# Optimization experiments

Hardware: AMD Instinct MI355X
Metric: run time of the kernel (lower is better)

Reference implementation:

```python
import jax, jax.numpy as jnp
import numpy as np

B, T, D = 8, 4096, 512
Q, K = 4, 1024
KERNEL, STRIDE = 5, 2
COMMIT = 0.25


def setup_inputs() -> dict:
    key = jax.random.key(0)
    k1, k2, k3 = jax.random.split(key, 3)
    x = jax.random.normal(k1, (B, T, D), dtype=jnp.float32)
    codebooks = jax.random.normal(k2, (Q, K, D), dtype=jnp.float32)
    # he_normal fan_in = KERNEL * D
    conv_w = jax.random.normal(k3, (KERNEL, D, D), dtype=jnp.float32) * np.sqrt(2.0 / (KERNEL * D))
    return {"x": x, "codebooks": codebooks, "conv_w": conv_w}


def _vq_nearest(residual, cb):
    # residual: [B,T,D], cb: [K,D] -> squared L2 distances [B,T,K]
    d = (jnp.sum(residual * residual, axis=-1, keepdims=True)
         - 2.0 * jnp.einsum('btd,kd->btk', residual, cb)
         + jnp.sum(cb * cb, axis=-1))
    idx = jnp.argmin(d, axis=-1)          # [B,T] int
    q = cb[idx]                            # [B,T,D] gather
    return q, idx


def residual_vq(x, codebooks):
    residual = x
    quantized_out = jnp.zeros_like(x)
    losses = []
    indices = []
    for qi in range(Q):  # small fixed number of quantizers
        q, idx = _vq_nearest(residual, codebooks[qi])
        # commitment loss (codebook frozen at inference / EMA-updated in training)
        losses.append(COMMIT * jnp.mean((jax.lax.stop_gradient(q) - residual) ** 2))
        # straight-through estimator
        q_st = residual + jax.lax.stop_gradient(q - residual)
        quantized_out = quantized_out + q_st
        residual = residual - jax.lax.stop_gradient(q)
        indices.append(idx)
    loss = jnp.sum(jnp.stack(losses))
    return quantized_out, jnp.stack(indices, axis=0), loss


def reference(x, codebooks, conv_w):
    quantized_out, indices, vq_loss = residual_vq(x, codebooks)
    # Conv1D, stride 2, 'same' padding, no bias: NWC x WIO -> NWC
    y = jax.lax.conv_general_dilated(
        quantized_out, conv_w,
        window_strides=(STRIDE,), padding='SAME',
        dimension_numbers=('NWC', 'WIO', 'NWC'))
    y = jax.nn.gelu(y, approximate=False)
    return y, quantized_out, indices, vq_loss
```

## Files before the change

kernel.cpp:

```cpp
#include <hip/hip_runtime.h>
#include <math.h>

#define Bq 8
#define Tq 4096
#define Dq 512
#define Qn 4
#define Kk 1024
#define OWn 2048
#define NROWS (Bq*Tq)

#define QO_OFF (Bq*OWn*Dq)
#define IDX_OFF (QO_OFF + Bq*Tq*Dq)
#define LOSS_OFF (IDX_OFF + Qn*NROWS)

typedef __bf16 bf16x8 __attribute__((ext_vector_type(8)));
typedef _Float16 f16x8 __attribute__((ext_vector_type(8)));
typedef float f32x16 __attribute__((ext_vector_type(16)));
typedef float f32x4 __attribute__((ext_vector_type(4)));

__device__ __forceinline__ unsigned pack2h(_Float16 a, _Float16 b) {
  return (unsigned)__builtin_bit_cast(unsigned short, a)
       | ((unsigned)__builtin_bit_cast(unsigned short, b) << 16);
}

__global__ __launch_bounds__(256) void prep_cb(const float* __restrict__ cb,
                                               float* __restrict__ cbnorm,
                                               _Float16* __restrict__ cbf,
                                               float* __restrict__ lacc) {
  int w = threadIdx.x >> 6, lane = threadIdx.x & 63;
  int row = blockIdx.x * 4 + w;
  int q = row >> 10, k = row & 1023;
  const f32x4* c4 = (const f32x4*)(cb + (size_t)row * Dq);
  f32x4 v0 = c4[lane * 2], v1 = c4[lane * 2 + 1];
  float s = v0.x*v0.x + v0.y*v0.y + v0.z*v0.z + v0.w*v0.w
          + v1.x*v1.x + v1.y*v1.y + v1.z*v1.z + v1.w*v1.w;
  f16x8 bv;
  bv[0]=(_Float16)v0.x; bv[1]=(_Float16)v0.y; bv[2]=(_Float16)v0.z; bv[3]=(_Float16)v0.w;
  bv[4]=(_Float16)v1.x; bv[5]=(_Float16)v1.y; bv[6]=(_Float16)v1.z; bv[7]=(_Float16)v1.w;
  int ds = lane >> 1, hs = lane & 1;
  size_t off = ((size_t)((k >> 5) * 32 + ds) * 2 + hs) * 256 + (k & 31) * 8;
  *(f16x8*)(cbf + (size_t)q * (Kk * Dq) + off) = bv;
#pragma unroll
  for (int off2 = 32; off2; off2 >>= 1) s += __shfl_down(s, off2);
  if (lane == 0) cbnorm[row] = s;
  if (blockIdx.x == 0 && threadIdx.x == 0) *lacc = 0.f;
}

__global__ __launch_bounds__(256) void prep_cmax(const float* __restrict__ cbnorm,
                                                 float* __restrict__ cmax) {
  int w = threadIdx.x >> 6, lane = threadIdx.x & 63;
  float m = 0.f;
#pragma unroll
  for (int j = 0; j < 16; ++j) m = fmaxf(m, cbnorm[w * Kk + lane * 16 + j]);
#pragma unroll
  for (int off = 32; off; off >>= 1) m = fmaxf(m, __shfl_down(m, off));
  if (lane == 0) cmax[w] = sqrtf(m);
}

__global__ __launch_bounds__(256) void prep_wb(const float* __restrict__ w,
                                               __bf16* __restrict__ wb) {
  int g = blockIdx.x * 256 + threadIdx.x;
  int l31 = g & 31, hs = (g >> 5) & 1, c32 = (g >> 6) & 15, s = g >> 10;
  int kw = s >> 5, ci16 = s & 31;
  int ci = ci16 * 16 + hs * 8;
  int co = c32 * 32 + l31;
  bf16x8 bv;
#pragma unroll
  for (int e = 0; e < 8; ++e)
    bv[e] = (__bf16)w[(size_t)(kw * Dq + ci + e) * Dq + co];
  *(bf16x8*)(wb + (size_t)g * 8) = bv;
}

__global__ __launch_bounds__(512, 1) void vq_all(
    const float* __restrict__ x, float* __restrict__ qo,
    const _Float16* __restrict__ cbf, const float* __restrict__ cb,
    const float* __restrict__ cbnorm, const float* __restrict__ cmax,
    float* __restrict__ idxo, float* __restrict__ lacc) {
  __shared__ _Float16 rh[64 * 512];
  __shared__ unsigned redB[64 * 8];
  __shared__ float rnorm_l[64];
  __shared__ float thrL[64];
  __shared__ int rowcount[64];
  __shared__ unsigned short rowlist[64 * 32];

  const int tid = threadIdx.x;
  const int w = tid >> 6, lane = tid & 63, l31 = lane & 31, hs = lane >> 5;
  const int row0g = blockIdx.x * 64;
  char* rhc = (char*)rh;

  f32x4 r0[8], r1[8];
#pragma unroll
  for (int rr = 0; rr < 8; ++rr) {
    size_t gb = (size_t)(row0g + w * 8 + rr) * Dq + lane * 8;
    r0[rr] = *(const f32x4*)(x + gb);
    r1[rr] = *(const f32x4*)(x + gb + 4);
  }
  float lsum = 0.f;

#pragma unroll 1
  for (int qi = 0; qi < Qn; ++qi) {
    const _Float16* cbf_q = cbf + (size_t)qi * (Kk * Dq);
    const float*    cb_q  = cb  + (size_t)qi * (Kk * Dq);
    const float*    cbn_q = cbnorm + qi * Kk;

#pragma unroll
    for (int rr = 0; rr < 8; ++rr) {
      int row = w * 8 + rr;
      f16x8 bv;
      bv[0]=(_Float16)r0[rr].x; bv[1]=(_Float16)r0[rr].y;
      bv[2]=(_Float16)r0[rr].z; bv[3]=(_Float16)r0[rr].w;
      bv[4]=(_Float16)r1[rr].x; bv[5]=(_Float16)r1[rr].y;
      bv[6]=(_Float16)r1[rr].z; bv[7]=(_Float16)r1[rr].w;
      *(f16x8*)(rhc + ((row * 1024 + lane * 16) ^ ((row & 7) << 4))) = bv;
      float rn = r0[rr].x*r0[rr].x + r0[rr].y*r0[rr].y + r0[rr].z*r0[rr].z + r0[rr].w*r0[rr].w
               + r1[rr].x*r1[rr].x + r1[rr].y*r1[rr].y + r1[rr].z*r1[rr].z + r1[rr].w*r1[rr].w;
#pragma unroll
      for (int off = 1; off < 64; off <<= 1) rn += __shfl_xor(rn, off);
      if (lane == 0) rnorm_l[row] = rn;
    }
    __syncthreads();

    unsigned psA[4][8], psB[4][8];
    const int ab0 = l31 * 1024 + hs * 16;
    const int asw = (l31 & 7) << 4;
#pragma unroll
    for (int p = 0; p < 2; ++p) {
      const int ct0 = 2 * p, ct1 = 2 * p + 1;
      const _Float16* bp0 = cbf_q + (size_t)(w * 4 + ct0) * 16384 + hs * 256 + l31 * 8;
      const _Float16* bp1 = cbf_q + (size_t)(w * 4 + ct1) * 16384 + hs * 256 + l31 * 8;
      f32x16 a00, a01, a10, a11;
#pragma unroll
      for (int i = 0; i < 16; ++i) { a00[i]=0.f; a01[i]=0.f; a10[i]=0.f; a11[i]=0.f; }
#pragma unroll 8
      for (int ds = 0; ds < 32; ++ds) {
        f16x8 a0 = *(const f16x8*)(rhc + ((ab0 + ds * 32) ^ asw));
        f16x8 a1 = *(const f16x8*)(rhc + ((ab0 + 32 * 1024 + ds * 32) ^ asw));
        f16x8 b0 = *(const f16x8*)(bp0 + ds * 512);
        f16x8 b1 = *(const f16x8*)(bp1 + ds * 512);
        a00 = __builtin_amdgcn_mfma_f32_32x32x16_f16(a0, b0, a00, 0, 0, 0);
        a01 = __builtin_amdgcn_mfma_f32_32x32x16_f16(a0, b1, a01, 0, 0, 0);
        a10 = __builtin_amdgcn_mfma_f32_32x32x16_f16(a1, b0, a10, 0, 0, 0);
        a11 = __builtin_amdgcn_mfma_f32_32x32x16_f16(a1, b1, a11, 0, 0, 0);
      }
      const float cn0 = cbn_q[w * 128 + ct0 * 32 + l31];
      const float cn1 = cbn_q[w * 128 + ct1 * 32 + l31];
#pragma unroll
      for (int j = 0; j < 8; ++j) {
        psA[ct0][j] = pack2h((_Float16)(cn0 - 2.f * a00[2*j]), (_Float16)(cn0 - 2.f * a00[2*j+1]));
        psA[ct1][j] = pack2h((_Float16)(cn1 - 2.f * a01[2*j]), (_Float16)(cn1 - 2.f * a01[2*j+1]));
        psB[ct0][j] = pack2h((_Float16)(cn0 - 2.f * a10[2*j]), (_Float16)(cn0 - 2.f * a10[2*j+1]));
        psB[ct1][j] = pack2h((_Float16)(cn1 - 2.f * a11[2*j]), (_Float16)(cn1 - 2.f * a11[2*j+1]));
      }
    }

#pragma unroll
    for (int rt = 0; rt < 2; ++rt) {
      unsigned pk[16];
#pragma unroll
      for (int i = 0; i < 16; ++i) {
        pk[i] = 0xFFFFFFFFu;
#pragma unroll
        for (int ct = 0; ct < 4; ++ct) {
          unsigned col = (unsigned)(w * 128 + ct * 32 + l31);
          unsigned u = ((rt == 0 ? psA[ct][i >> 1] : psB[ct][i >> 1]) >> ((i & 1) * 16)) & 0xFFFFu;
          unsigned key = (u & 0x8000u) ? (u ^ 0xFFFFu) : (u | 0x8000u);
          unsigned pkc = (key << 10) | col;
          if (pkc < pk[i]) pk[i] = pkc;
        }
#pragma unroll
        for (int off = 1; off <= 16; off <<= 1) {
          unsigned t = __shfl_xor(pk[i], off);
          if (t < pk[i]) pk[i] = t;
        }
      }
      if (l31 == 0) {
#pragma unroll
        for (int i = 0; i < 16; ++i) {
          int rit = rt * 32 + (i & 3) + 8 * (i >> 2) + 4 * hs;
          redB[rit * 8 + w] = pk[i];
        }
      }
    }
    __syncthreads();

    if (tid < 64) {
      unsigned mb = redB[tid * 8];
#pragma unroll
      for (int j = 1; j < 8; ++j) {
        unsigned v = redB[tid * 8 + j];
        if (v < mb) mb = v;
      }
      unsigned key = (mb >> 10) & 0xFFFFu;
      unsigned ub = (key & 0x8000u) ? (key ^ 0x8000u) : (key ^ 0xFFFFu);
      float mstar = (float)__builtin_bit_cast(_Float16, (unsigned short)ub);
      float rn = sqrtf(rnorm_l[tid]);
      float cm = cmax[qi];
      thrL[tid] = mstar + 0.005f * rn * cm + 0.001f * fabsf(mstar) + 0.3f;
      rowcount[tid] = 0;
    }
    __syncthreads();

#pragma unroll
    for (int rt = 0; rt < 2; ++rt) {
#pragma unroll
      for (int i = 0; i < 16; ++i) {
        int rit = rt * 32 + (i & 3) + 8 * (i >> 2) + 4 * hs;
        float t = thrL[rit];
#pragma unroll
        for (int ct = 0; ct < 4; ++ct) {
          unsigned col = (unsigned)(w * 128 + ct * 32 + l31);
          unsigned u = ((rt == 0 ? psA[ct][i >> 1] : psB[ct][i >> 1]) >> ((i & 1) * 16)) & 0xFFFFu;
          float s = (float)__builtin_bit_cast(_Float16, (unsigned short)u);
          if (s <= t) {
            int p = atomicAdd(&rowcount[rit], 1);
            if (p < 32) rowlist[rit * 32 + p] = (unsigned short)col;
          }
        }
      }
    }
    __syncthreads();

#pragma unroll
    for (int rr = 0; rr < 8; ++rr) {
      int row = w * 8 + rr;
      int cnt = rowcount[row];
      int bk;
      if (cnt == 1) {
        bk = (int)rowlist[row * 32];
      } else {
        int total = (cnt > 32) ? Kk : cnt;
        float bs = 3.4028235e38f; bk = 1 << 30;
        for (int ci2 = 0; ci2 < total; ++ci2) {
          int k = (cnt > 32) ? ci2 : (int)rowlist[row * 32 + ci2];
          const f32x4* crow = (const f32x4*)(cb_q + ((size_t)k << 9)) + lane * 2;
          f32x4 c0 = crow[0], c1 = crow[1];
          float dot = 0.f;
          dot = fmaf(r0[rr].x, c0.x, dot); dot = fmaf(r0[rr].y, c0.y, dot);
          dot = fmaf(r0[rr].z, c0.z, dot); dot = fmaf(r0[rr].w, c0.w, dot);
          dot = fmaf(r1[rr].x, c1.x, dot); dot = fmaf(r1[rr].y, c1.y, dot);
          dot = fmaf(r1[rr].z, c1.z, dot); dot = fmaf(r1[rr].w, c1.w, dot);
#pragma unroll
          for (int off = 1; off < 64; off <<= 1) dot += __shfl_xor(dot, off);
          float sc = cbn_q[k] - 2.f * dot;
          if (sc < bs || (sc == bs && k < bk)) { bs = sc; bk = k; }
        }
      }
      if (lane == 0) idxo[(size_t)qi * NROWS + row0g + row] = (float)bk;
      const f32x4* crow = (const f32x4*)(cb_q + ((size_t)bk << 9)) + lane * 2;
      f32x4 c0 = crow[0], c1 = crow[1];
      r0[rr].x -= c0.x; r0[rr].y -= c0.y; r0[rr].z -= c0.z; r0[rr].w -= c0.w;
      r1[rr].x -= c1.x; r1[rr].y -= c1.y; r1[rr].z -= c1.z; r1[rr].w -= c1.w;
      lsum += r0[rr].x*r0[rr].x + r0[rr].y*r0[rr].y + r0[rr].z*r0[rr].z + r0[rr].w*r0[rr].w
            + r1[rr].x*r1[rr].x + r1[rr].y*r1[rr].y + r1[rr].z*r1[rr].z + r1[rr].w*r1[rr].w;
    }
    __syncthreads();
  }

#pragma unroll
  for (int rr = 0; rr < 8; ++rr) {
    size_t gb = (size_t)(row0g + w * 8 + rr) * Dq + lane * 8;
    f32x4 xv0 = *(const f32x4*)(x + gb), xv1 = *(const f32x4*)(x + gb + 4);
    f32x4 o0, o1;
    o0.x = xv0.x - r0[rr].x; o0.y = xv0.y - r0[rr].y;
    o0.z = xv0.z - r0[rr].z; o0.w = xv0.w - r0[rr].w;
    o1.x = xv1.x - r1[rr].x; o1.y = xv1.y - r1[rr].y;
    o1.z = xv1.z - r1[rr].z; o1.w = xv1.w - r1[rr].w;
    *(f32x4*)(qo + gb) = o0;
    *(f32x4*)(qo + gb + 4) = o1;
  }
#pragma unroll
  for (int off = 1; off < 64; off <<= 1) lsum += __shfl_xor(lsum, off);
  if (lane == 0) atomicAdd(lacc, lsum);
}

__global__ __launch_bounds__(512, 2) void conv_mfma(const float* __restrict__ qo,
                                                    const __bf16* __restrict__ wb,
                                                    float* __restrict__ y) {
  __shared__ char As[259 * 128];
  const int tid = threadIdx.x;
  const int w = tid >> 6, lane = tid & 63, l31 = lane & 31, hs = lane >> 5;
  const int rowblk = blockIdx.x, coblk = blockIdx.y;
  const int n = rowblk >> 4;
  const int o0 = (rowblk & 15) * 128;
  const int t0 = 2 * o0 - 1;
  const int c32g = coblk * 8 + w;

  f32x16 acc[4];
#pragma unroll
  for (int rt = 0; rt < 4; ++rt)
#pragma unroll
    for (int i = 0; i < 16; ++i) acc[rt][i] = 0.f;

  for (int ct8 = 0; ct8 < 8; ++ct8) {
    __syncthreads();
    for (int s = tid; s < 2072; s += 512) {
      int irow = s >> 3, cg = s & 7;
      int t = t0 + irow;
      bf16x8 bv;
      if (t >= 0 && t < Tq) {
        const float* src = qo + ((size_t)(n * Tq + t)) * Dq + ct8 * 64 + cg * 8;
        f32x4 v0 = *(const f32x4*)(src), v1 = *(const f32x4*)(src + 4);
        bv[0]=(__bf16)v0.x; bv[1]=(__bf16)v0.y; bv[2]=(__bf16)v0.z; bv[3]=(__bf16)v0.w;
        bv[4]=(__bf16)v1.x; bv[5]=(__bf16)v1.y; bv[6]=(__bf16)v1.z; bv[7]=(__bf16)v1.w;
      } else {
#pragma unroll
        for (int e = 0; e < 8; ++e) bv[e] = (__bf16)0.f;
      }
      *(bf16x8*)(As + ((irow * 128 + cg * 16) ^ (((irow >> 1) & 7) << 4))) = bv;
    }
    __syncthreads();
#pragma unroll
    for (int kw = 0; kw < 5; ++kw) {
#pragma unroll
      for (int ks = 0; ks < 4; ++ks) {
        int s16 = kw * 32 + ct8 * 4 + ks;
        bf16x8 b = *(const bf16x8*)(wb + ((size_t)(s16 * 16 + c32g) * 2 + hs) * 256 + l31 * 8);
#pragma unroll
        for (int rt = 0; rt < 4; ++rt) {
          int ir = 2 * (rt * 32 + l31) + kw;
          bf16x8 a = *(const bf16x8*)(As + ((ir * 128 + ks * 32 + hs * 16) ^ (((ir >> 1) & 7) << 4)));
          acc[rt] = __builtin_amdgcn_mfma_f32_32x32x16_bf16(a, b, acc[rt], 0, 0, 0);
        }
      }
    }
  }
  const int co = coblk * 256 + w * 32 + l31;
#pragma unroll
  for (int rt = 0; rt < 4; ++rt)
#pragma unroll
    for (int i = 0; i < 16; ++i) {
      int orow = rt * 32 + (i & 3) + 8 * (i >> 2) + 4 * hs;
      float v = acc[rt][i];
      float g = 0.5f * v * (1.f + erff(v * 0.70710678118654752f));
      y[((size_t)(n * OWn + o0 + orow)) * Dq + co] = g;
    }
}

__global__ void loss_final(const float* __restrict__ lacc, float* __restrict__ out) {
  out[0] = 0.25f * lacc[0] / 16777216.0f;
}

extern "C" void kernel_launch(void* const* d_in, const int* in_sizes, int n_in,
                              void* d_out, int out_size, void* d_ws, size_t ws_size,
                              hipStream_t stream) {
  const float* x  = (const float*)d_in[0];
  const float* cb = (const float*)d_in[1];
  const float* cw = (const float*)d_in[2];
  float* out = (float*)d_out;
  float* y    = out;
  float* qo   = out + QO_OFF;
  float* idxo = out + IDX_OFF;
  float* losso = out + LOSS_OFF;

  float* fws    = (float*)d_ws;
  float* lacc   = fws;
  float* cmax   = fws + 8;
  float* cbnorm = fws + 16;
  _Float16* cbf = (_Float16*)((char*)d_ws + (32 << 10));
  __bf16* wb  = (__bf16*)((char*)d_ws + (8 << 20));

  prep_cb<<<1024, 256, 0, stream>>>(cb, cbnorm, cbf, lacc);
  prep_cmax<<<1, 256, 0, stream>>>(cbnorm, cmax);
  prep_wb<<<640, 256, 0, stream>>>(cw, wb);

  vq_all<<<512, 512, 0, stream>>>(x, qo, cbf, cb, cbnorm, cmax, idxo, lacc);

  conv_mfma<<<dim3(128, 2), 512, 0, stream>>>(qo, wb, y);
  loss_final<<<1, 1, 0, stream>>>(lacc, losso);
}
```

Before: 478.5 us.

## Recompute distance GEMM in second pass instead of holding packed scores in registers

Replaces the stored 64 packed-half score registers and the packed-key argmin reduction with a running packed-f16 min per row, followed by a second full MFMA pass that recomputes the scores for candidate thresholding. This cuts register pressure and the key-packing ALU work, but doubles the codebook-distance matmul work and the codebook loads per quantizer. The thresholding now compares fp32 scores rather than the f16-rounded ones.

```diff
diff --git a/kernel.cpp b/kernel.cpp
--- a/kernel.cpp
+++ b/kernel.cpp
@@ -21,6 +21,15 @@
 __device__ __forceinline__ unsigned pack2h(_Float16 a, _Float16 b) {
   return (unsigned)__builtin_bit_cast(unsigned short, a)
        | ((unsigned)__builtin_bit_cast(unsigned short, b) << 16);
+}
+__device__ __forceinline__ unsigned pmin2h(unsigned a, unsigned b) {
+  _Float16 al = __builtin_bit_cast(_Float16, (unsigned short)(a & 0xFFFFu));
+  _Float16 ah = __builtin_bit_cast(_Float16, (unsigned short)(a >> 16));
+  _Float16 bl = __builtin_bit_cast(_Float16, (unsigned short)(b & 0xFFFFu));
+  _Float16 bh = __builtin_bit_cast(_Float16, (unsigned short)(b >> 16));
+  _Float16 ml = al < bl ? al : bl;
+  _Float16 mh = ah < bh ? ah : bh;
+  return pack2h(ml, mh);
 }
 
 __global__ __launch_bounds__(256) void prep_cb(const float* __restrict__ cb,
@@ -77,7 +86,7 @@
     const float* __restrict__ cbnorm, const float* __restrict__ cmax,
     float* __restrict__ idxo, float* __restrict__ lacc) {
   __shared__ _Float16 rh[64 * 512];
-  __shared__ unsigned redB[64 * 8];
+  __shared__ float minW[64 * 8];
   __shared__ float rnorm_l[64];
   __shared__ float thrL[64];
   __shared__ int rowcount[64];
@@ -120,101 +129,94 @@
     }
     __syncthreads();
 
-    unsigned psA[4][8], psB[4][8];
     const int ab0 = l31 * 1024 + hs * 16;
+    const int ab1 = ab0 + 32 * 1024;
     const int asw = (l31 & 7) << 4;
-#pragma unroll
-    for (int p = 0; p < 2; ++p) {
-      const int ct0 = 2 * p, ct1 = 2 * p + 1;
-      const _Float16* bp0 = cbf_q + (size_t)(w * 4 + ct0) * 16384 + hs * 256 + l31 * 8;
-      const _Float16* bp1 = cbf_q + (size_t)(w * 4 + ct1) * 16384 + hs * 256 + l31 * 8;
-      f32x16 a00, a01, a10, a11;
-#pragma unroll
-      for (int i = 0; i < 16; ++i) { a00[i]=0.f; a01[i]=0.f; a10[i]=0.f; a11[i]=0.f; }
+
+    unsigned minp[16];
+#pragma unroll
+    for (int i = 0; i < 16; ++i) minp[i] = 0x7C007C00u;
+
+#pragma unroll 1
+    for (int ct = 0; ct < 4; ++ct) {
+      const int col = w * 128 + ct * 32 + l31;
+      const _Float16* bp = cbf_q + (size_t)(w * 4 + ct) * 16384 + hs * 256 + l31 * 8;
+      f32x16 acc0, acc1;
+#pragma unroll
+      for (int i = 0; i < 16; ++i) { acc0[i] = 0.f; acc1[i] = 0.f; }
 #pragma unroll 8
       for (int ds = 0; ds < 32; ++ds) {
         f16x8 a0 = *(const f16x8*)(rhc + ((ab0 + ds * 32) ^ asw));
-        f16x8 a1 = *(const f16x8*)(rhc + ((ab0 + 32 * 1024 + ds * 32) ^ asw));
-        f16x8 b0 = *(const f16x8*)(bp0 + ds * 512);
-        f16x8 b1 = *(const f16x8*)(bp1 + ds * 512);
-        a00 = __builtin_amdgcn_mfma_f32_32x32x16_f16(a0, b0, a00, 0, 0, 0);
-        a01 = __builtin_amdgcn_mfma_f32_32x32x16_f16(a0, b1, a01, 0, 0, 0);
-        a10 = __builtin_amdgcn_mfma_f32_32x32x16_f16(a1, b0, a10, 0, 0, 0);
-        a11 = __builtin_amdgcn_mfma_f32_32x32x16_f16(a1, b1, a11, 0, 0, 0);
-      }
-      const float cn0 = cbn_q[w * 128 + ct0 * 32 + l31];
-      const float cn1 = cbn_q[w * 128 + ct1 * 32 + l31];
-#pragma unroll
-      for (int j = 0; j < 8; ++j) {
-        psA[ct0][j] = pack2h((_Float16)(cn0 - 2.f * a00[2*j]), (_Float16)(cn0 - 2.f * a00[2*j+1]));
-        psA[ct1][j] = pack2h((_Float16)(cn1 - 2.f * a01[2*j]), (_Float16)(cn1 - 2.f * a01[2*j+1]));
-        psB[ct0][j] = pack2h((_Float16)(cn0 - 2.f * a10[2*j]), (_Float16)(cn0 - 2.f * a10[2*j+1]));
-        psB[ct1][j] = pack2h((_Float16)(cn1 - 2.f * a11[2*j]), (_Float16)(cn1 - 2.f * a11[2*j+1]));
-      }
-    }
-
-#pragma unroll
-    for (int rt = 0; rt < 2; ++rt) {
-      unsigned pk[16];
+        f16x8 a1 = *(const f16x8*)(rhc + ((ab1 + ds * 32) ^ asw));
+        f16x8 b  = *(const f16x8*)(bp + ds * 512);
+        acc0 = __builtin_amdgcn_mfma_f32_32x32x16_f16(a0, b, acc0, 0, 0, 0);
+        acc1 = __builtin_amdgcn_mfma_f32_32x32x16_f16(a1, b, acc1, 0, 0, 0);
+      }
+      const float cn = cbn_q[col];
 #pragma unroll
       for (int i = 0; i < 16; ++i) {
-        pk[i] = 0xFFFFFFFFu;
-#pragma unroll
-        for (int ct = 0; ct < 4; ++ct) {
-          unsigned col = (unsigned)(w * 128 + ct * 32 + l31);
-          unsigned u = ((rt == 0 ? psA[ct][i >> 1] : psB[ct][i >> 1]) >> ((i & 1) * 16)) & 0xFFFFu;
-          unsigned key = (u & 0x8000u) ? (u ^ 0xFFFFu) : (u | 0x8000u);
-          unsigned pkc = (key << 10) | col;
-          if (pkc < pk[i]) pk[i] = pkc;
-        }
-#pragma unroll
-        for (int off = 1; off <= 16; off <<= 1) {
-          unsigned t = __shfl_xor(pk[i], off);
-          if (t < pk[i]) pk[i] = t;
-        }
-      }
-      if (l31 == 0) {
-#pragma unroll
-        for (int i = 0; i < 16; ++i) {
-          int rit = rt * 32 + (i & 3) + 8 * (i >> 2) + 4 * hs;
-          redB[rit * 8 + w] = pk[i];
-        }
+        _Float16 h0 = (_Float16)(cn - 2.f * acc0[i]);
+        _Float16 h1 = (_Float16)(cn - 2.f * acc1[i]);
+        minp[i] = pmin2h(minp[i], pack2h(h0, h1));
+      }
+    }
+#pragma unroll
+    for (int i = 0; i < 16; ++i) {
+#pragma unroll
+      for (int off = 1; off <= 16; off <<= 1)
+        minp[i] = pmin2h(minp[i], __shfl_xor(minp[i], off));
+    }
+    if (l31 == 0) {
+#pragma unroll
+      for (int i = 0; i < 16; ++i) {
+        int rit = (i & 3) + 8 * (i >> 2) + 4 * hs;
+        minW[rit * 8 + w] =
+            (float)__builtin_bit_cast(_Float16, (unsigned short)(minp[i] & 0xFFFFu));
+        minW[(rit + 32) * 8 + w] =
+            (float)__builtin_bit_cast(_Float16, (unsigned short)(minp[i] >> 16));
       }
     }
     __syncthreads();
 
     if (tid < 64) {
-      unsigned mb = redB[tid * 8];
-#pragma unroll
-      for (int j = 1; j < 8; ++j) {
-        unsigned v = redB[tid * 8 + j];
-        if (v < mb) mb = v;
-      }
-      unsigned key = (mb >> 10) & 0xFFFFu;
-      unsigned ub = (key & 0x8000u) ? (key ^ 0x8000u) : (key ^ 0xFFFFu);
-      float mstar = (float)__builtin_bit_cast(_Float16, (unsigned short)ub);
+      float m = minW[tid * 8];
+#pragma unroll
+      for (int j = 1; j < 8; ++j) m = fminf(m, minW[tid * 8 + j]);
       float rn = sqrtf(rnorm_l[tid]);
       float cm = cmax[qi];
-      thrL[tid] = mstar + 0.005f * rn * cm + 0.001f * fabsf(mstar) + 0.3f;
+      thrL[tid] = m + 0.005f * rn * cm + 0.001f * fabsf(m) + 0.3f;
       rowcount[tid] = 0;
     }
     __syncthreads();
 
-#pragma unroll
-    for (int rt = 0; rt < 2; ++rt) {
+#pragma unroll 1
+    for (int ct = 0; ct < 4; ++ct) {
+      const int col = w * 128 + ct * 32 + l31;
+      const _Float16* bp = cbf_q + (size_t)(w * 4 + ct) * 16384 + hs * 256 + l31 * 8;
+      f32x16 acc0, acc1;
+#pragma unroll
+      for (int i = 0; i < 16; ++i) { acc0[i] = 0.f; acc1[i] = 0.f; }
+#pragma unroll 8
+      for (int ds = 0; ds < 32; ++ds) {
+        f16x8 a0 = *(const f16x8*)(rhc + ((ab0 + ds * 32) ^ asw));
+        f16x8 a1 = *(const f16x8*)(rhc + ((ab1 + ds * 32) ^ asw));
+        f16x8 b  = *(const f16x8*)(bp + ds * 512);
+        acc0 = __builtin_amdgcn_mfma_f32_32x32x16_f16(a0, b, acc0, 0, 0, 0);
+        acc1 = __builtin_amdgcn_mfma_f32_32x32x16_f16(a1, b, acc1, 0, 0, 0);
+      }
+      const float cn = cbn_q[col];
 #pragma unroll
       for (int i = 0; i < 16; ++i) {
-        int rit = rt * 32 + (i & 3) + 8 * (i >> 2) + 4 * hs;
-        float t = thrL[rit];
-#pragma unroll
-        for (int ct = 0; ct < 4; ++ct) {
-          unsigned col = (unsigned)(w * 128 + ct * 32 + l31);
-          unsigned u = ((rt == 0 ? psA[ct][i >> 1] : psB[ct][i >> 1]) >> ((i & 1) * 16)) & 0xFFFFu;
-          float s = (float)__builtin_bit_cast(_Float16, (unsigned short)u);
-          if (s <= t) {
-            int p = atomicAdd(&rowcount[rit], 1);
-            if (p < 32) rowlist[rit * 32 + p] = (unsigned short)col;
-          }
+        int rit = (i & 3) + 8 * (i >> 2) + 4 * hs;
+        float s0 = cn - 2.f * acc0[i];
+        float s1 = cn - 2.f * acc1[i];
+        if (s0 <= thrL[rit]) {
+          int p = atomicAdd(&rowcount[rit], 1);
+          if (p < 32) rowlist[rit * 32 + p] = (unsigned short)col;
+        }
+        if (s1 <= thrL[rit + 32]) {
+          int p = atomicAdd(&rowcount[rit + 32], 1);
+          if (p < 32) rowlist[(rit + 32) * 32 + p] = (unsigned short)col;
         }
       }
     }
```

Measured after the change: 531.5 us. 1.11x slower.

## Stream residual through global qo instead of holding it in registers; split MFMA tiles

Applied to the files above, without the earlier changes.

Drops the 64 per-thread registers that held the residual across all quantizer passes. Each pass now recomputes the residual as x minus the running quantized sum, which is read back from and written to the qo output in global memory. The distance MMA is also restructured to run the two row tiles one after another, so only two 16-wide accumulators are live instead of four. The aim is to cut register pressure, likely to avoid spills or free VGPRs, at the cost of extra global reads and writes of x and qo on every pass.

```diff
diff --git a/kernel.cpp b/kernel.cpp
--- a/kernel.cpp
+++ b/kernel.cpp
@@ -87,14 +87,6 @@
   const int w = tid >> 6, lane = tid & 63, l31 = lane & 31, hs = lane >> 5;
   const int row0g = blockIdx.x * 64;
   char* rhc = (char*)rh;
-
-  f32x4 r0[8], r1[8];
-#pragma unroll
-  for (int rr = 0; rr < 8; ++rr) {
-    size_t gb = (size_t)(row0g + w * 8 + rr) * Dq + lane * 8;
-    r0[rr] = *(const f32x4*)(x + gb);
-    r1[rr] = *(const f32x4*)(x + gb + 4);
-  }
   float lsum = 0.f;
 
 #pragma unroll 1
@@ -103,17 +95,26 @@
     const float*    cb_q  = cb  + (size_t)qi * (Kk * Dq);
     const float*    cbn_q = cbnorm + qi * Kk;
 
-#pragma unroll
+#pragma unroll 1
     for (int rr = 0; rr < 8; ++rr) {
       int row = w * 8 + rr;
+      size_t gb = (size_t)(row0g + row) * Dq + lane * 8;
+      f32x4 xv0 = *(const f32x4*)(x + gb), xv1 = *(const f32x4*)(x + gb + 4);
+      f32x4 qv0 = {0.f,0.f,0.f,0.f}, qv1 = {0.f,0.f,0.f,0.f};
+      if (qi != 0) { qv0 = *(const f32x4*)(qo + gb); qv1 = *(const f32x4*)(qo + gb + 4); }
+      f32x4 rv0, rv1;
+      rv0.x = xv0.x - qv0.x; rv0.y = xv0.y - qv0.y;
+      rv0.z = xv0.z - qv0.z; rv0.w = xv0.w - qv0.w;
+      rv1.x = xv1.x - qv1.x; rv1.y = xv1.y - qv1.y;
+      rv1.z = xv1.z - qv1.z; rv1.w = xv1.w - qv1.w;
       f16x8 bv;
-      bv[0]=(_Float16)r0[rr].x; bv[1]=(_Float16)r0[rr].y;
-      bv[2]=(_Float16)r0[rr].z; bv[3]=(_Float16)r0[rr].w;
-      bv[4]=(_Float16)r1[rr].x; bv[5]=(_Float16)r1[rr].y;
-      bv[6]=(_Float16)r1[rr].z; bv[7]=(_Float16)r1[rr].w;
+      bv[0]=(_Float16)rv0.x; bv[1]=(_Float16)rv0.y;
+      bv[2]=(_Float16)rv0.z; bv[3]=(_Float16)rv0.w;
+      bv[4]=(_Float16)rv1.x; bv[5]=(_Float16)rv1.y;
+      bv[6]=(_Float16)rv1.z; bv[7]=(_Float16)rv1.w;
       *(f16x8*)(rhc + ((row * 1024 + lane * 16) ^ ((row & 7) << 4))) = bv;
-      float rn = r0[rr].x*r0[rr].x + r0[rr].y*r0[rr].y + r0[rr].z*r0[rr].z + r0[rr].w*r0[rr].w
-               + r1[rr].x*r1[rr].x + r1[rr].y*r1[rr].y + r1[rr].z*r1[rr].z + r1[rr].w*r1[rr].w;
+      float rn = rv0.x*rv0.x + rv0.y*rv0.y + rv0.z*rv0.z + rv0.w*rv0.w
+               + rv1.x*rv1.x + rv1.y*rv1.y + rv1.z*rv1.z + rv1.w*rv1.w;
 #pragma unroll
       for (int off = 1; off < 64; off <<= 1) rn += __shfl_xor(rn, off);
       if (lane == 0) rnorm_l[row] = rn;
@@ -128,28 +129,31 @@
       const int ct0 = 2 * p, ct1 = 2 * p + 1;
       const _Float16* bp0 = cbf_q + (size_t)(w * 4 + ct0) * 16384 + hs * 256 + l31 * 8;
       const _Float16* bp1 = cbf_q + (size_t)(w * 4 + ct1) * 16384 + hs * 256 + l31 * 8;
-      f32x16 a00, a01, a10, a11;
-#pragma unroll
-      for (int i = 0; i < 16; ++i) { a00[i]=0.f; a01[i]=0.f; a10[i]=0.f; a11[i]=0.f; }
-#pragma unroll 8
-      for (int ds = 0; ds < 32; ++ds) {
-        f16x8 a0 = *(const f16x8*)(rhc + ((ab0 + ds * 32) ^ asw));
-        f16x8 a1 = *(const f16x8*)(rhc + ((ab0 + 32 * 1024 + ds * 32) ^ asw));
-        f16x8 b0 = *(const f16x8*)(bp0 + ds * 512);
-        f16x8 b1 = *(const f16x8*)(bp1 + ds * 512);
-        a00 = __builtin_amdgcn_mfma_f32_32x32x16_f16(a0, b0, a00, 0, 0, 0);
-        a01 = __builtin_amdgcn_mfma_f32_32x32x16_f16(a0, b1, a01, 0, 0, 0);
-        a10 = __builtin_amdgcn_mfma_f32_32x32x16_f16(a1, b0, a10, 0, 0, 0);
-        a11 = __builtin_amdgcn_mfma_f32_32x32x16_f16(a1, b1, a11, 0, 0, 0);
-      }
       const float cn0 = cbn_q[w * 128 + ct0 * 32 + l31];
       const float cn1 = cbn_q[w * 128 + ct1 * 32 + l31];
 #pragma unroll
-      for (int j = 0; j < 8; ++j) {
-        psA[ct0][j] = pack2h((_Float16)(cn0 - 2.f * a00[2*j]), (_Float16)(cn0 - 2.f * a00[2*j+1]));
-        psA[ct1][j] = pack2h((_Float16)(cn1 - 2.f * a01[2*j]), (_Float16)(cn1 - 2.f * a01[2*j+1]));
-        psB[ct0][j] = pack2h((_Float16)(cn0 - 2.f * a10[2*j]), (_Float16)(cn0 - 2.f * a10[2*j+1]));
-        psB[ct1][j] = pack2h((_Float16)(cn1 - 2.f * a11[2*j]), (_Float16)(cn1 - 2.f * a11[2*j+1]));
+      for (int rt = 0; rt < 2; ++rt) {
+        f32x16 acc0, acc1;
+#pragma unroll
+        for (int i = 0; i < 16; ++i) { acc0[i] = 0.f; acc1[i] = 0.f; }
+        const int abase = ab0 + rt * 32768;
+#pragma unroll 8
+        for (int ds = 0; ds < 32; ++ds) {
+          f16x8 a  = *(const f16x8*)(rhc + ((abase + ds * 32) ^ asw));
+          f16x8 b0 = *(const f16x8*)(bp0 + ds * 512);
+          f16x8 b1 = *(const f16x8*)(bp1 + ds * 512);
+          acc0 = __builtin_amdgcn_mfma_f32_32x32x16_f16(a, b0, acc0, 0, 0, 0);
+          acc1 = __builtin_amdgcn_mfma_f32_32x32x16_f16(a, b1, acc1, 0, 0, 0);
+        }
+#pragma unroll
+        for (int j = 0; j < 8; ++j) {
+          unsigned v0 = pack2h((_Float16)(cn0 - 2.f * acc0[2*j]),
+                               (_Float16)(cn0 - 2.f * acc0[2*j+1]));
+          unsigned v1 = pack2h((_Float16)(cn1 - 2.f * acc1[2*j]),
+                               (_Float16)(cn1 - 2.f * acc1[2*j+1]));
+          if (rt == 0) { psA[ct0][j] = v0; psA[ct1][j] = v1; }
+          else         { psB[ct0][j] = v0; psB[ct1][j] = v1; }
+        }
       }
     }
 
@@ -220,9 +224,18 @@
     }
     __syncthreads();
 
-#pragma unroll
+#pragma unroll 1
     for (int rr = 0; rr < 8; ++rr) {
       int row = w * 8 + rr;
+      size_t gb = (size_t)(row0g + row) * Dq + lane * 8;
+      f32x4 xv0 = *(const f32x4*)(x + gb), xv1 = *(const f32x4*)(x + gb + 4);
+      f32x4 qv0 = {0.f,0.f,0.f,0.f}, qv1 = {0.f,0.f,0.f,0.f};
+      if (qi != 0) { qv0 = *(const f32x4*)(qo + gb); qv1 = *(const f32x4*)(qo + gb + 4); }
+      f32x4 rv0, rv1;
+      rv0.x = xv0.x - qv0.x; rv0.y = xv0.y - qv0.y;
+      rv0.z = xv0.z - qv0.z; rv0.w = xv0.w - qv0.w;
+      rv1.x = xv1.x - qv1.x; rv1.y = xv1.y - qv1.y;
+      rv1.z = xv1.z - qv1.z; rv1.w = xv1.w - qv1.w;
       int cnt = rowcount[row];
       int bk;
       if (cnt == 1) {
@@ -235,10 +248,10 @@
           const f32x4* crow = (const f32x4*)(cb_q + ((size_t)k << 9)) + lane * 2;
           f32x4 c0 = crow[0], c1 = crow[1];
           float dot = 0.f;
-          dot = fmaf(r0[rr].x, c0.x, dot); dot = fmaf(r0[rr].y, c0.y, dot);
-          dot = fmaf(r0[rr].z, c0.z, dot); dot = fmaf(r0[rr].w, c0.w, dot);
-          dot = fmaf(r1[rr].x, c1.x, dot); dot = fmaf(r1[rr].y, c1.y, dot);
-          dot = fmaf(r1[rr].z, c1.z, dot); dot = fmaf(r1[rr].w, c1.w, dot);
+          dot = fmaf(rv0.x, c0.x, dot); dot = fmaf(rv0.y, c0.y, dot);
+          dot = fmaf(rv0.z, c0.z, dot); dot = fmaf(rv0.w, c0.w, dot);
+          dot = fmaf(rv1.x, c1.x, dot); dot = fmaf(rv1.y, c1.y, dot);
+          dot = fmaf(rv1.z, c1.z, dot); dot = fmaf(rv1.w, c1.w, dot);
 #pragma unroll
           for (int off = 1; off < 64; off <<= 1) dot += __shfl_xor(dot, off);
           float sc = cbn_q[k] - 2.f * dot;
@@ -248,26 +261,20 @@
       if (lane == 0) idxo[(size_t)qi * NROWS + row0g + row] = (float)bk;
       const f32x4* crow = (const f32x4*)(cb_q + ((size_t)bk << 9)) + lane * 2;
       f32x4 c0 = crow[0], c1 = crow[1];
-      r0[rr].x -= c0.x; r0[rr].y -= c0.y; r0[rr].z -= c0.z; r0[rr].w -= c0.w;
-      r1[rr].x -= c1.x; r1[rr].y -= c1.y; r1[rr].z -= c1.z; r1[rr].w -= c1.w;
-      lsum += r0[rr].x*r0[rr].x + r0[rr].y*r0[rr].y + r0[rr].z*r0[rr].z + r0[rr].w*r0[rr].w
-            + r1[rr].x*r1[rr].x + r1[rr].y*r1[rr].y + r1[rr].z*r1[rr].z + r1[rr].w*r1[rr].w;
+      f32x4 n0, n1;
+      n0.x = qv0.x + c0.x; n0.y = qv0.y + c0.y;
+      n0.z = qv0.z + c0.z; n0.w = qv0.w + c0.w;
+      n1.x = qv1.x + c1.x; n1.y = qv1.y + c1.y;
+      n1.z = qv1.z + c1.z; n1.w = qv1.w + c1.w;
+      *(f32x4*)(qo + gb) = n0;
+      *(f32x4*)(qo + gb + 4) = n1;
+      float a0 = xv0.x - n0.x, a1 = xv0.y - n0.y, a2 = xv0.z - n0.z, a3 = xv0.w - n0.w;
+      float a4 = xv1.x - n1.x, a5 = xv1.y - n1.y, a6 = xv1.z - n1.z, a7 = xv1.w - n1.w;
+      lsum += a0*a0 + a1*a1 + a2*a2 + a3*a3 + a4*a4 + a5*a5 + a6*a6 + a7*a7;
     }
     __syncthreads();
   }
 
-#pragma unroll
-  for (int rr = 0; rr < 8; ++rr) {
-    size_t gb = (size_t)(row0g + w * 8 + rr) * Dq + lane * 8;
-    f32x4 xv0 = *(const f32x4*)(x + gb), xv1 = *(const f32x4*)(x + gb + 4);
-    f32x4 o0, o1;
-    o0.x = xv0.x - r0[rr].x; o0.y = xv0.y - r0[rr].y;
-    o0.z = xv0.z - r0[rr].z; o0.w = xv0.w - r0[rr].w;
-    o1.x = xv1.x - r1[rr].x; o1.y = xv1.y - r1[rr].y;
-    o1.z = xv1.z - r1[rr].z; o1.w = xv1.w - r1[rr].w;
-    *(f32x4*)(qo + gb) = o0;
-    *(f32x4*)(qo + gb + 4) = o1;
-  }
 #pragma unroll
   for (int off = 1; off < 64; off <<= 1) lsum += __shfl_xor(lsum, off);
   if (lane == 0) atomicAdd(lacc, lsum);
```

Result: slower. 553.9 us (+15.7%).
